# Kernel tuning notes

Hardware: AMD Instinct MI355X
Metric: run time of the kernel (lower is better)

## Reference

```python
import jax, jax.numpy as jnp
import numpy as np

D_MODEL = 1024
N_HEADS = 16
NUM_KV_HEADS = 4
D_K = D_MODEL // N_HEADS
ROPE_BASE = 10000.0


def apply_rotary_emb(x, base):
    # x: (B, H, T, d) ; rotate interleaved pairs (x[2i], x[2i+1])
    B, H, T, d = x.shape
    inv_freq = 1.0 / (base ** (jnp.arange(0, d, 2, dtype=jnp.float32) / d))  # (d/2,)
    angles = jnp.arange(T, dtype=jnp.float32)[:, None] * inv_freq[None, :]   # (T, d/2)
    cos = jnp.cos(angles)[None, None]  # (1,1,T,d/2)
    sin = jnp.sin(angles)[None, None]
    x1 = x[..., 0::2]
    x2 = x[..., 1::2]
    out = jnp.stack([x1 * cos - x2 * sin, x1 * sin + x2 * cos], axis=-1)
    return out.reshape(B, H, T, d)


def setup_inputs() -> dict:
    key = jax.random.key(0)
    k1, k2, k3, k4, k5 = jax.random.split(key, 5)
    B, T = 4, 2048
    s = 1.0 / np.sqrt(D_MODEL)
    return {
        "x": jax.random.normal(k1, (B, T, D_MODEL), dtype=jnp.float32),
        "attention_mask": jnp.ones((B, T), dtype=jnp.int32),
        "Wq": jax.random.uniform(k2, (D_MODEL, D_MODEL), jnp.float32, -s, s),
        "Wk": jax.random.uniform(k3, (D_MODEL, NUM_KV_HEADS * D_K), jnp.float32, -s, s),
        "Wv": jax.random.uniform(k4, (D_MODEL, NUM_KV_HEADS * D_K), jnp.float32, -s, s),
        "Wo": jax.random.uniform(k5, (D_MODEL, D_MODEL), jnp.float32, -s, s),
    }


def reference(x, attention_mask, Wq, Wk, Wv, Wo):
    B, T, _ = x.shape
    # QKV projections -> (B, H, T, d_k)
    Q = (x @ Wq).reshape(B, T, N_HEADS, D_K).transpose(0, 2, 1, 3)
    K = (x @ Wk).reshape(B, T, NUM_KV_HEADS, D_K).transpose(0, 2, 1, 3)
    V = (x @ Wv).reshape(B, T, NUM_KV_HEADS, D_K).transpose(0, 2, 1, 3)
    # RoPE on Q and K
    Q = apply_rotary_emb(Q, ROPE_BASE)
    K = apply_rotary_emb(K, ROPE_BASE)
    # GQA expansion: repeat kv heads to match query heads
    rep = N_HEADS // NUM_KV_HEADS
    K = jnp.repeat(K, rep, axis=1)
    V = jnp.repeat(V, rep, axis=1)
    # mask: causal AND query-position padding (faithful to source's pad[:,None,:,None])
    causal = jnp.tril(jnp.ones((T, T), dtype=bool))[None, None]        # (1,1,T,T)
    pad = attention_mask.astype(bool)[:, None, :, None]                 # (B,1,T,1)
    mask = pad & causal                                                 # (B,1,T,T)
    scale = 1.0 / np.sqrt(D_K)
    scores = jnp.einsum("bhqd,bhkd->bhqk", Q, K) * scale
    scores = jnp.where(mask, scores, jnp.finfo(scores.dtype).min)
    attn = jax.nn.softmax(scores, axis=-1)
    out = jnp.einsum("bhqk,bhkd->bhqd", attn, V)                       # (B,H,T,d_k)
    out = out.transpose(0, 2, 1, 3).reshape(B, T, D_MODEL)
    return out @ Wo
```

## Files before the change

kernel.cpp:

```cpp
#include <hip/hip_runtime.h>
#include <hip/hip_bf16.h>


#define B_   4
#define T_   2048
#define DM   1024
#define NH   16
#define NKV  4
#define DK   64
#define BT   (B_ * T_)
#define DKV  (NKV * DK)

typedef __attribute__((ext_vector_type(4))) short s4;
typedef __attribute__((ext_vector_type(8))) short s8;
typedef __attribute__((ext_vector_type(4))) float f4;
typedef __attribute__((ext_vector_type(16))) float f16x;

#define L2E    1.4426950408889634f
#define L2_1E4 0.41524101186092307f

__device__ __forceinline__ unsigned short f2bf(float f) {
    __hip_bfloat16 h = __float2bfloat16(f);
    unsigned short u; __builtin_memcpy(&u, &h, 2); return u;
}
__device__ __forceinline__ float bf2f(unsigned short u) {
    __hip_bfloat16 h; __builtin_memcpy(&h, &u, 2); return __bfloat162float(h);
}

__device__ __forceinline__ float ldf(const void* p, size_t i, bool f32) {
    return f32 ? ((const float*)p)[i]
               : __bfloat162float(((const __hip_bfloat16*)p)[i]);
}
__device__ __forceinline__ bool world_f32(const int* flag) {
    return __builtin_amdgcn_readfirstlane(flag[0]) == 0;
}

__device__ __forceinline__ void async_cp16(const unsigned short* g, unsigned short* l) {
    __builtin_amdgcn_global_load_lds(
        (const __attribute__((address_space(1))) void*)g,
        (__attribute__((address_space(3))) void*)l,
        16, 0, 0);
}

__global__ void probe_fmt(const unsigned int* __restrict__ x, int* __restrict__ flag)
{
    __shared__ int cnt;
    if (threadIdx.x == 0) cnt = 0;
    __syncthreads();
    int local = 0;
    #pragma unroll
    for (int i = 0; i < 16; ++i) {
        unsigned int w  = x[threadIdx.x * 16 + i];
        unsigned int lo = w & 0xFFFFu;
        unsigned int e  = (lo >> 7) & 0xFFu;
        if ((lo & 0x7FFFu) == 0u || (e >= 96u && e <= 144u)) ++local;
    }
    atomicAdd(&cnt, local);
    __syncthreads();
    if (threadIdx.x == 0) flag[0] = (cnt >= 3072) ? 1 : 0;
}

__global__ __launch_bounds__(256) void cvt_x(const float* __restrict__ x,
                                             unsigned short* __restrict__ xb,
                                             const int* __restrict__ flag)
{
    if (!world_f32(flag)) return;
    const size_t i = ((size_t)blockIdx.x * 256 + threadIdx.x) * 8;
    f4 a = *(const f4*)(x + i);
    f4 b = *(const f4*)(x + i + 4);
    unsigned short h[8] = { f2bf(a.x), f2bf(a.y), f2bf(a.z), f2bf(a.w),
                            f2bf(b.x), f2bf(b.y), f2bf(b.z), f2bf(b.w) };
    __builtin_memcpy(xb + i, h, 16);
}

__global__ __launch_bounds__(256) void transp2(const void* __restrict__ W0,
                                               const void* __restrict__ W1,
                                               unsigned short* __restrict__ T0,
                                               unsigned short* __restrict__ T1,
                                               int K, int N,
                                               const int* __restrict__ flag)
{
    const bool f32 = world_f32(flag);
    __shared__ unsigned short Tl[32][33];
    const void* W = blockIdx.z ? W1 : W0;
    unsigned short* T = blockIdx.z ? T1 : T0;
    const int n0 = blockIdx.x * 32, k0 = blockIdx.y * 32;
    const int tx = threadIdx.x & 31, ty = threadIdx.x >> 5;
    #pragma unroll
    for (int i = 0; i < 4; ++i)
        Tl[ty + 8 * i][tx] = f2bf(ldf(W, (size_t)(k0 + ty + 8 * i) * N + n0 + tx, f32));
    __syncthreads();
    #pragma unroll
    for (int i = 0; i < 4; ++i)
        T[(size_t)(n0 + ty + 8 * i) * K + k0 + tx] = Tl[tx][ty + 8 * i];
}

__global__ __launch_bounds__(256) void gemm_bt(const unsigned short* __restrict__ A0,
                                               const unsigned short* __restrict__ A1,
                                               const unsigned short* __restrict__ Bt,
                                               void* __restrict__ C,
                                               void* __restrict__ C2,
                                               int M, int N, int K,
                                               const int* __restrict__ flag,
                                               int mode,
                                               int rope_mode, float rope_scale)
{
    const unsigned short* Ab = world_f32(flag) ? A1 : A0;

    __shared__ unsigned short Al[2][128 * 64];
    __shared__ unsigned short Bl[2][128 * 64];

    const int tid  = threadIdx.x;
    const int bm   = blockIdx.y * 128;
    const int bn   = blockIdx.x * 128;
    const int w    = tid >> 6;
    const int lane = tid & 63;
    const int qd   = lane >> 4;
    const int ln   = lane & 15;
    const int wm   = (w & 1) * 64;
    const int wn   = (w >> 1) * 64;
    const int sr   = tid >> 2;
    const int sk   = (tid & 3) * 8;

#define STAGE(bf, k0_) {                                                              \
    async_cp16(Ab + (size_t)(bm + sr) * K + (k0_) + sk,           &Al[bf][tid * 8]);         \
    async_cp16(Ab + (size_t)(bm + 64 + sr) * K + (k0_) + sk,      &Al[bf][2048 + tid * 8]);  \
    async_cp16(Ab + (size_t)(bm + sr) * K + (k0_) + 32 + sk,      &Al[bf][4096 + tid * 8]);  \
    async_cp16(Ab + (size_t)(bm + 64 + sr) * K + (k0_) + 32 + sk, &Al[bf][6144 + tid * 8]);  \
    async_cp16(Bt + (size_t)(bn + sr) * K + (k0_) + sk,           &Bl[bf][tid * 8]);         \
    async_cp16(Bt + (size_t)(bn + 64 + sr) * K + (k0_) + sk,      &Bl[bf][2048 + tid * 8]);  \
    async_cp16(Bt + (size_t)(bn + sr) * K + (k0_) + 32 + sk,      &Bl[bf][4096 + tid * 8]);  \
    async_cp16(Bt + (size_t)(bn + 64 + sr) * K + (k0_) + 32 + sk, &Bl[bf][6144 + tid * 8]);  \
}

    f4 zero = {0.f, 0.f, 0.f, 0.f};
    f4 acc[4][4];
    #pragma unroll
    for (int i = 0; i < 4; ++i)
        #pragma unroll
        for (int j = 0; j < 4; ++j) acc[i][j] = zero;

    const int NS = K >> 6;
    STAGE(0, 0)
    for (int s = 0; s < NS; ++s) {
        const int cur = s & 1;
        if (s + 1 < NS) {
            STAGE(cur ^ 1, (s + 1) << 6)
            asm volatile("s_waitcnt vmcnt(16)" ::: "memory");
        } else {
            asm volatile("s_waitcnt vmcnt(0)" ::: "memory");
        }
        asm volatile("s_barrier" ::: "memory");

        #pragma unroll
        for (int ks = 0; ks < 2; ++ks) {
            s8 af[4], bfr[4];
            #pragma unroll
            for (int i = 0; i < 4; ++i)
                af[i] = *(const s8*)&Al[cur][ks * 4096 + (wm + 16 * i + ln) * 32 + qd * 8];
            #pragma unroll
            for (int j = 0; j < 4; ++j)
                bfr[j] = *(const s8*)&Bl[cur][ks * 4096 + (wn + 16 * j + ln) * 32 + qd * 8];
            #pragma unroll
            for (int i = 0; i < 4; ++i)
                #pragma unroll
                for (int j = 0; j < 4; ++j)
                    acc[i][j] = __builtin_amdgcn_mfma_f32_16x16x32_bf16(af[i], bfr[j], acc[i][j], 0, 0, 0);
        }
        asm volatile("s_barrier" ::: "memory");
    }
#undef STAGE

    if (rope_mode) {
        #pragma unroll
        for (int j = 0; j < 4; ++j) {
            const int col = bn + wn + 16 * j + ln;
            const bool do_rope = (rope_mode == 1) || (col < 256);
            if (do_rope) {
                const int pr = (col >> 1) & 31;
                const float invf = exp2f(-(float)pr * L2_1E4);
                const bool odd = col & 1;
                #pragma unroll
                for (int i = 0; i < 4; ++i)
                    #pragma unroll
                    for (int r = 0; r < 4; ++r) {
                        const int row = bm + wm + 16 * i + qd * 4 + r;
                        float v = acc[i][j][r];
                        float pv = __shfl_xor(v, 1);
                        float ang = (float)(row & (T_ - 1)) * invf;
                        float sn, cs;
                        __sincosf(ang, &sn, &cs);
                        float out = odd ? (pv * sn + v * cs) : (v * cs - pv * sn);
                        acc[i][j][r] = out * rope_scale;
                    }
            }
        }
    }

    #pragma unroll
    for (int i = 0; i < 4; ++i)
        #pragma unroll
        for (int r = 0; r < 4; ++r) {
            const int row = bm + wm + 16 * i + qd * 4 + r;
            #pragma unroll
            for (int j = 0; j < 4; ++j) {
                const int col = bn + wn + 16 * j + ln;
                const float v = acc[i][j][r];
                if (mode == 0) {
                    ((unsigned short*)C)[(size_t)row * N + col] = f2bf(v);
                } else {
                    unsigned short* dst = (unsigned short*)(col < 256 ? C : C2);
                    dst[(size_t)row * 256 + (col & 255)] = f2bf(v);
                }
            }
        }
}

__global__ __launch_bounds__(256, 3) void attn_mfma(unsigned short* __restrict__ QO,
                                                    const unsigned short* __restrict__ Kg,
                                                    const unsigned short* __restrict__ Vg)
{
    __shared__ unsigned short Kl[64][72];
    __shared__ unsigned short Vl[64][72];

    const int ip   = blockIdx.x;
    const int bh   = blockIdx.y;
    const int b    = bh >> 4;
    const int h    = bh & 15;
    const int hkv  = h >> 2;
    const int tid  = threadIdx.x;
    const int w    = tid >> 6;
    const int lane = tid & 63;
    const int q    = lane & 31;
    const int hl   = lane >> 5;

    const int rk = tid >> 2, dk = (tid & 3) * 16;
    const int kp = tid & 31, vd0 = (tid >> 5) * 8;
    const unsigned short* kptr = Kg + (size_t)(b * T_ + rk) * DKV + hkv * DK + dk;
    const unsigned short* vptr = Vg + (size_t)(b * T_ + 2 * kp) * DKV + hkv * DK + vd0;

    #pragma unroll 1
    for (int seg = 0; seg < 2; ++seg) {
        const int qt    = seg ? ip : (15 - ip);
        const int qb    = qt * 128;
        const int ktmax = 2 * qt + 1;

        uint4 kra0 = ((const uint4*)kptr)[0];
        uint4 kra1 = ((const uint4*)kptr)[1];
        uint4 vra0 = *(const uint4*)vptr;
        uint4 vra1 = *(const uint4*)(vptr + DKV);

        s8 qf[4];
        {
            const unsigned short* Qp =
                QO + (size_t)(b * T_ + qb + 32 * w + q) * DM + h * DK + 8 * hl;
            #pragma unroll
            for (int s = 0; s < 4; ++s)
                qf[s] = *(const s8*)(Qp + 16 * s);
        }

        const int qmaxw = qb + 32 * w + 31;
        const int qglob = qb + 32 * w + q;

        f16x O0, O1;
        #pragma unroll
        for (int r = 0; r < 16; ++r) { O0[r] = 0.f; O1[r] = 0.f; }
        float lsumA = 0.f, lsumB = 0.f;

        for (int kt = 0; kt <= ktmax; ++kt) {
            *(uint4*)&Kl[rk][dk]     = kra0;
            *(uint4*)&Kl[rk][dk + 8] = kra1;
            {
                const unsigned short* lo = (const unsigned short*)&vra0;
                const unsigned short* hi = (const unsigned short*)&vra1;
                #pragma unroll
                for (int i = 0; i < 8; ++i)
                    *(unsigned int*)&Vl[vd0 + i][2 * kp] =
                        (unsigned int)lo[i] | ((unsigned int)hi[i] << 16);
            }
            if (kt < ktmax) {
                const size_t o = (size_t)(kt + 1) * 64 * DKV;
                kra0 = ((const uint4*)(kptr + o))[0];
                kra1 = ((const uint4*)(kptr + o))[1];
                vra0 = *(const uint4*)(vptr + o);
                vra1 = *(const uint4*)(vptr + o + DKV);
            }
            asm volatile("s_waitcnt lgkmcnt(0)\n\ts_barrier" ::: "memory");

            const int kb = kt * 64;
            if (kb <= qmaxw) {
                f16x S0, S1;
                #pragma unroll
                for (int r = 0; r < 16; ++r) { S0[r] = 0.f; S1[r] = 0.f; }
                #pragma unroll
                for (int s = 0; s < 4; ++s) {
                    s8 k0 = *(const s8*)&Kl[q][16 * s + 8 * hl];
                    s8 k1 = *(const s8*)&Kl[32 + q][16 * s + 8 * hl];
                    S0 = __builtin_amdgcn_mfma_f32_32x32x16_bf16(k0, qf[s], S0, 0, 0, 0);
                    S1 = __builtin_amdgcn_mfma_f32_32x32x16_bf16(k1, qf[s], S1, 0, 0, 0);
                }

                unsigned pk0[8], pk1[8];
                const bool full = (kb + 63 <= qb + 32 * w);
                if (full) {
                    #pragma unroll
                    for (int j = 0; j < 8; ++j) {
                        float a0 = exp2f(S0[2 * j]), a1 = exp2f(S0[2 * j + 1]);
                        float c0 = exp2f(S1[2 * j]), c1 = exp2f(S1[2 * j + 1]);
                        lsumA += a0 + a1;
                        lsumB += c0 + c1;
                        pk0[j] = (unsigned)f2bf(a0) | ((unsigned)f2bf(a1) << 16);
                        pk1[j] = (unsigned)f2bf(c0) | ((unsigned)f2bf(c1) << 16);
                    }
                } else {
                    #pragma unroll
                    for (int j = 0; j < 8; ++j) {
                        const int r0 = 2 * j;
                        const int key0 = kb + (r0 & 3) + 8 * (r0 >> 2) + 4 * hl;
                        float a0 = (key0      <= qglob) ? exp2f(S0[r0])     : 0.f;
                        float a1 = (key0 + 1  <= qglob) ? exp2f(S0[r0 + 1]) : 0.f;
                        float c0 = (key0 + 32 <= qglob) ? exp2f(S1[r0])     : 0.f;
                        float c1 = (key0 + 33 <= qglob) ? exp2f(S1[r0 + 1]) : 0.f;
                        lsumA += a0 + a1;
                        lsumB += c0 + c1;
                        pk0[j] = (unsigned)f2bf(a0) | ((unsigned)f2bf(a1) << 16);
                        pk1[j] = (unsigned)f2bf(c0) | ((unsigned)f2bf(c1) << 16);
                    }
                }

                #define PV_STEP(PG, KS) {                                          \
                    const unsigned a0 = PG[4 * ((KS) & 1) + 0];                    \
                    const unsigned a1 = PG[4 * ((KS) & 1) + 1];                    \
                    const unsigned a2 = PG[4 * ((KS) & 1) + 2];                    \
                    const unsigned a3 = PG[4 * ((KS) & 1) + 3];                    \
                    const unsigned own0 = hl ? a2 : a0;                            \
                    const unsigned own1 = hl ? a3 : a1;                            \
                    const unsigned xs0  = hl ? a0 : a2;                            \
                    const unsigned xs1  = hl ? a1 : a3;                            \
                    const unsigned xa = (unsigned)__shfl_xor((int)xs0, 32);        \
                    const unsigned xb = (unsigned)__shfl_xor((int)xs1, 32);        \
                    unsigned dw[4];                                                \
                    dw[0] = hl ? xa : own0;                                        \
                    dw[1] = hl ? xb : own1;                                        \
                    dw[2] = hl ? own0 : xa;                                        \
                    dw[3] = hl ? own1 : xb;                                        \
                    s8 pf; __builtin_memcpy(&pf, dw, 16);                          \
                    s8 v0 = *(const s8*)&Vl[q][16 * (KS) + 8 * hl];                \
                    s8 v1 = *(const s8*)&Vl[32 + q][16 * (KS) + 8 * hl];           \
                    O0 = __builtin_amdgcn_mfma_f32_32x32x16_bf16(v0, pf, O0, 0, 0, 0); \
                    O1 = __builtin_amdgcn_mfma_f32_32x32x16_bf16(v1, pf, O1, 0, 0, 0); \
                }
                PV_STEP(pk0, 0)
                PV_STEP(pk0, 1)
                PV_STEP(pk1, 2)
                PV_STEP(pk1, 3)
                #undef PV_STEP
            }
            asm volatile("s_barrier" ::: "memory");
        }

        const float lsum = lsumA + lsumB;
        const float lf = lsum + __shfl_xor(lsum, 32);
        const float inv = 1.0f / lf;
        unsigned short* Op = QO + (size_t)(b * T_ + qb + 32 * w + q) * DM + h * DK;
        #pragma unroll
        for (int g2 = 0; g2 < 2; ++g2) {
            #pragma unroll
            for (int rq = 0; rq < 4; ++rq) {
                const int d0 = 32 * g2 + 8 * rq + 4 * hl;
                const float o0 = (g2 ? O1[4 * rq + 0] : O0[4 * rq + 0]) * inv;
                const float o1 = (g2 ? O1[4 * rq + 1] : O0[4 * rq + 1]) * inv;
                const float o2 = (g2 ? O1[4 * rq + 2] : O0[4 * rq + 2]) * inv;
                const float o3 = (g2 ? O1[4 * rq + 3] : O0[4 * rq + 3]) * inv;
                unsigned out2[2] = {
                    (unsigned)f2bf(o0) | ((unsigned)f2bf(o1) << 16),
                    (unsigned)f2bf(o2) | ((unsigned)f2bf(o3) << 16) };
                __builtin_memcpy(Op + d0, out2, 8);
            }
        }
    }
}

__global__ __launch_bounds__(256) void copy_out(const unsigned short* __restrict__ Cb,
                                                void* __restrict__ out,
                                                const int* __restrict__ flag)
{
    const bool f32 = world_f32(flag);
    size_t i = ((size_t)blockIdx.x * 256 + threadIdx.x) * 8;
    uint4 v = *(const uint4*)(Cb + i);
    if (!f32) {
        *(uint4*)((unsigned short*)out + i) = v;
    } else {
        const unsigned short* u = (const unsigned short*)&v;
        float* o = (float*)out + i;
        #pragma unroll
        for (int k = 0; k < 8; ++k) o[k] = bf2f(u[k]);
    }
}

extern "C" void kernel_launch(void* const* d_in, const int* in_sizes, int n_in,
                              void* d_out, int out_size, void* d_ws, size_t ws_size,
                              hipStream_t stream)
{
    const void* x  = d_in[0];
    const void* Wq = d_in[2];
    const void* Wk = d_in[3];
    const void* Wv = d_in[4];
    const void* Wo = d_in[5];

    int* flag = (int*)d_ws;
    unsigned short* WqT  = (unsigned short*)((char*)d_ws + 4096);
    unsigned short* WkvT = WqT + (size_t)DM * DM;
    unsigned short* WoT  = WkvT + (size_t)512 * DM;
    unsigned short* Kb   = WoT + (size_t)DM * DM;
    unsigned short* Vb   = Kb + (size_t)BT * DKV;
    unsigned short* Cb   = Kb;

    unsigned short* Qb = (unsigned short*)d_out;
    unsigned short* xb = (unsigned short*)d_out + (size_t)BT * DM;

    dim3 blk(256);

    probe_fmt<<<1, blk, 0, stream>>>((const unsigned int*)x, flag);

    cvt_x<<<dim3(BT * DM / 2048), blk, 0, stream>>>((const float*)x, xb, flag);

    transp2<<<dim3(32, 32, 2), blk, 0, stream>>>(Wq, Wo, WqT, WoT, DM, DM, flag);
    transp2<<<dim3(8, 32, 2), blk, 0, stream>>>(Wk, Wv, WkvT, WkvT + (size_t)256 * DM, DM, DKV, flag);

    gemm_bt<<<dim3(DM / 128, BT / 128), blk, 0, stream>>>(
        (const unsigned short*)x, xb, WqT, Qb, nullptr, BT, DM, DM, flag, 0, 1, 0.125f * L2E);
    gemm_bt<<<dim3(512 / 128, BT / 128), blk, 0, stream>>>(
        (const unsigned short*)x, xb, WkvT, Kb, Vb, BT, 512, DM, flag, 2, 2, 1.0f);

    attn_mfma<<<dim3(T_ / 256, B_ * NH), blk, 0, stream>>>(Qb, Kb, Vb);

    gemm_bt<<<dim3(DM / 128, BT / 128), blk, 0, stream>>>(
        Qb, Qb, WoT, Cb, nullptr, BT, DM, DM, flag, 0, 0, 1.0f);
    copy_out<<<dim3(BT * DM / 2048), blk, 0, stream>>>(Cb, d_out, flag);
}
```

Baseline: 274.3 us.

## Triple-buffer GEMM with 32-wide K stages and XCD-aware block remapping

The GEMM pipeline changes from two 64-wide K stages to three 32-wide stages, keeping two loads in flight ahead of compute with a finer wait count. Both the GEMM and the attention kernel now remap block indices so consecutive workgroups spread across the eight XCDs, which groups tiles that share data on the same die for better L2 locality. Shared memory per GEMM block drops, but each stage does half the MFMA work between barriers, so synchronisation overhead per unit of work rises. The remap assumes the grid size is divisible by 8 and that the attention grid is 8 by 64.

```diff
diff --git a/kernel.cpp b/kernel.cpp
--- a/kernel.cpp
+++ b/kernel.cpp
@@ -107,12 +107,16 @@
 {
     const unsigned short* Ab = world_f32(flag) ? A1 : A0;
 
-    __shared__ unsigned short Al[2][128 * 64];
-    __shared__ unsigned short Bl[2][128 * 64];
+    __shared__ unsigned short Al[3][128 * 32];
+    __shared__ unsigned short Bl[3][128 * 32];
 
     const int tid  = threadIdx.x;
-    const int bm   = blockIdx.y * 128;
-    const int bn   = blockIdx.x * 128;
+    const int nwg = gridDim.x * gridDim.y;
+    const int lin = blockIdx.x + gridDim.x * blockIdx.y;
+    const int L   = (lin & 7) * (nwg >> 3) + (lin >> 3);
+    const int bm  = (L / gridDim.x) * 128;
+    const int bn  = (L % gridDim.x) * 128;
+
     const int w    = tid >> 6;
     const int lane = tid & 63;
     const int qd   = lane >> 4;
@@ -122,15 +126,11 @@
     const int sr   = tid >> 2;
     const int sk   = (tid & 3) * 8;
 
-#define STAGE(bf, k0_) {                                                              \
-    async_cp16(Ab + (size_t)(bm + sr) * K + (k0_) + sk,           &Al[bf][tid * 8]);         \
-    async_cp16(Ab + (size_t)(bm + 64 + sr) * K + (k0_) + sk,      &Al[bf][2048 + tid * 8]);  \
-    async_cp16(Ab + (size_t)(bm + sr) * K + (k0_) + 32 + sk,      &Al[bf][4096 + tid * 8]);  \
-    async_cp16(Ab + (size_t)(bm + 64 + sr) * K + (k0_) + 32 + sk, &Al[bf][6144 + tid * 8]);  \
-    async_cp16(Bt + (size_t)(bn + sr) * K + (k0_) + sk,           &Bl[bf][tid * 8]);         \
-    async_cp16(Bt + (size_t)(bn + 64 + sr) * K + (k0_) + sk,      &Bl[bf][2048 + tid * 8]);  \
-    async_cp16(Bt + (size_t)(bn + sr) * K + (k0_) + 32 + sk,      &Bl[bf][4096 + tid * 8]);  \
-    async_cp16(Bt + (size_t)(bn + 64 + sr) * K + (k0_) + 32 + sk, &Bl[bf][6144 + tid * 8]);  \
+#define STAGE(bb, k0_) {                                                                 \
+    async_cp16(Ab + (size_t)(bm + sr) * K + (k0_) + sk,      &Al[bb][tid * 8]);          \
+    async_cp16(Ab + (size_t)(bm + 64 + sr) * K + (k0_) + sk, &Al[bb][2048 + tid * 8]);   \
+    async_cp16(Bt + (size_t)(bn + sr) * K + (k0_) + sk,      &Bl[bb][tid * 8]);          \
+    async_cp16(Bt + (size_t)(bn + 64 + sr) * K + (k0_) + sk, &Bl[bb][2048 + tid * 8]);   \
 }
 
     f4 zero = {0.f, 0.f, 0.f, 0.f};
@@ -140,33 +140,28 @@
         #pragma unroll
         for (int j = 0; j < 4; ++j) acc[i][j] = zero;
 
-    const int NS = K >> 6;
+    const int NS = K >> 5;
     STAGE(0, 0)
+    if (NS > 1) STAGE(1, 32)
     for (int s = 0; s < NS; ++s) {
-        const int cur = s & 1;
-        if (s + 1 < NS) {
-            STAGE(cur ^ 1, (s + 1) << 6)
-            asm volatile("s_waitcnt vmcnt(16)" ::: "memory");
-        } else {
-            asm volatile("s_waitcnt vmcnt(0)" ::: "memory");
-        }
+        const int cur = s % 3;
+        if (s + 1 < NS) asm volatile("s_waitcnt vmcnt(4)" ::: "memory");
+        else            asm volatile("s_waitcnt vmcnt(0)" ::: "memory");
+        if (s + 2 < NS) { STAGE((s + 2) % 3, (s + 2) << 5) }
         asm volatile("s_barrier" ::: "memory");
 
-        #pragma unroll
-        for (int ks = 0; ks < 2; ++ks) {
-            s8 af[4], bfr[4];
-            #pragma unroll
-            for (int i = 0; i < 4; ++i)
-                af[i] = *(const s8*)&Al[cur][ks * 4096 + (wm + 16 * i + ln) * 32 + qd * 8];
+        s8 af[4], bfr[4];
+        #pragma unroll
+        for (int i = 0; i < 4; ++i)
+            af[i] = *(const s8*)&Al[cur][(wm + 16 * i + ln) * 32 + qd * 8];
+        #pragma unroll
+        for (int j = 0; j < 4; ++j)
+            bfr[j] = *(const s8*)&Bl[cur][(wn + 16 * j + ln) * 32 + qd * 8];
+        #pragma unroll
+        for (int i = 0; i < 4; ++i)
             #pragma unroll
             for (int j = 0; j < 4; ++j)
-                bfr[j] = *(const s8*)&Bl[cur][ks * 4096 + (wn + 16 * j + ln) * 32 + qd * 8];
-            #pragma unroll
-            for (int i = 0; i < 4; ++i)
-                #pragma unroll
-                for (int j = 0; j < 4; ++j)
-                    acc[i][j] = __builtin_amdgcn_mfma_f32_16x16x32_bf16(af[i], bfr[j], acc[i][j], 0, 0, 0);
-        }
+                acc[i][j] = __builtin_amdgcn_mfma_f32_16x16x32_bf16(af[i], bfr[j], acc[i][j], 0, 0, 0);
         asm volatile("s_barrier" ::: "memory");
     }
 #undef STAGE
@@ -223,8 +218,10 @@
     __shared__ unsigned short Kl[64][72];
     __shared__ unsigned short Vl[64][72];
 
-    const int ip   = blockIdx.x;
-    const int bh   = blockIdx.y;
+    const int lin = blockIdx.x + 8 * blockIdx.y;
+    const int L   = (lin & 7) * 64 + (lin >> 3);
+    const int ip  = L & 7;
+    const int bh  = L >> 3;
     const int b    = bh >> 4;
     const int h    = bh & 15;
     const int hkv  = h >> 2;
```

Result: slower. 281.7 us (+2.7%).
